# Performance work log

Hardware: AMD Instinct MI355X
Metric: run time of the kernel (lower is better)

Reference implementation:

```python
import jax, jax.numpy as jnp
import numpy as np

EPS = 1e-5

def conv1x1(x, w, b):
    # x: [B,C,H,W], w: [O,C], b: [O]
    return jnp.einsum('bchw,oc->bohw', x, w) + b[None, :, None, None]

def bn(x, g, b, m, v):
    # eval-mode BatchNorm2d over channel axis 1
    s = g / jnp.sqrt(v + EPS)
    return (x - m[None, :, None, None]) * s[None, :, None, None] + b[None, :, None, None]

def setup_inputs() -> dict:
    key = jax.random.key(0)
    ks = jax.random.split(key, 12)
    B, C, Ci, H, W = 8, 512, 256, 64, 64
    d = {}
    d['x'] = jax.random.normal(ks[0], (B, C, H, W), jnp.float32)
    d['theta_w'] = jax.random.normal(ks[1], (Ci, C), jnp.float32) * (C ** -0.5)
    d['theta_b'] = jnp.zeros((Ci,), jnp.float32)
    d['theta_bn_g'] = jax.random.uniform(ks[2], (Ci,), jnp.float32, 0.5, 1.5)
    d['theta_bn_b'] = jax.random.normal(ks[3], (Ci,), jnp.float32) * 0.1
    d['theta_bn_m'] = jnp.zeros((Ci,), jnp.float32)
    d['theta_bn_v'] = jnp.ones((Ci,), jnp.float32)
    d['phi_w'] = jax.random.normal(ks[4], (Ci, C), jnp.float32) * (C ** -0.5)
    d['phi_b'] = jnp.zeros((Ci,), jnp.float32)
    d['phi_bn_g'] = jax.random.uniform(ks[5], (Ci,), jnp.float32, 0.5, 1.5)
    d['phi_bn_b'] = jax.random.normal(ks[6], (Ci,), jnp.float32) * 0.1
    d['phi_bn_m'] = jnp.zeros((Ci,), jnp.float32)
    d['phi_bn_v'] = jnp.ones((Ci,), jnp.float32)
    d['g_w'] = jax.random.normal(ks[7], (Ci, C), jnp.float32) * (C ** -0.5)
    d['g_b'] = jnp.zeros((Ci,), jnp.float32)
    d['wz_w'] = jax.random.normal(ks[8], (C, Ci), jnp.float32) * (Ci ** -0.5)
    d['wz_b'] = jnp.zeros((C,), jnp.float32)
    d['wz_bn_g'] = jax.random.uniform(ks[9], (C,), jnp.float32, 0.5, 1.5)
    d['wz_bn_b'] = jax.random.normal(ks[10], (C,), jnp.float32) * 0.1
    d['wz_bn_m'] = jnp.zeros((C,), jnp.float32)
    d['wz_bn_v'] = jnp.ones((C,), jnp.float32)
    return d

def reference(x, theta_w, theta_b, theta_bn_g, theta_bn_b, theta_bn_m, theta_bn_v,
              phi_w, phi_b, phi_bn_g, phi_bn_b, phi_bn_m, phi_bn_v,
              g_w, g_b, wz_w, wz_b, wz_bn_g, wz_bn_b, wz_bn_m, wz_bn_v):
    B, C, H, W = x.shape
    Ci = theta_w.shape[0]
    N = H * W
    scale = Ci ** -0.5
    th = bn(conv1x1(x, theta_w, theta_b), theta_bn_g, theta_bn_b, theta_bn_m, theta_bn_v).reshape(B, Ci, N)
    ph = bn(conv1x1(x, phi_w, phi_b), phi_bn_g, phi_bn_b, phi_bn_m, phi_bn_v).reshape(B, Ci, N)
    gx = conv1x1(x, g_w, g_b).reshape(B, Ci, N)
    # attn[b,n,m] = <theta[:,n], phi[:,m]> * scale, softmax over m (fp32 as in source)
    attn = jax.nn.softmax(jnp.einsum('bcn,bcm->bnm', th, ph) * scale, axis=-1)
    y = jnp.einsum('bnm,bcm->bcn', attn, gx).reshape(B, Ci, H, W)
    out = bn(conv1x1(y, wz_w, wz_b), wz_bn_g, wz_bn_b, wz_bn_m, wz_bn_v) + x
    return out
```

## Files before the change

kernel.cpp:

```cpp
#include <hip/hip_runtime.h>

typedef __attribute__((ext_vector_type(8))) short bf16x8;
typedef __attribute__((ext_vector_type(4))) float f32x4;
typedef __attribute__((ext_vector_type(16))) float f32x16;
typedef __attribute__((ext_vector_type(4))) unsigned short us4;
typedef __attribute__((ext_vector_type(8))) unsigned short us8;
typedef __attribute__((ext_vector_type(4))) unsigned int u32x4;

#define B_  8
#define C_  512
#define CI_ 256
#define N_  4096

__device__ __forceinline__ unsigned short f2b(float f) {
  unsigned u = __float_as_uint(f);
  u += 0x7FFFu + ((u >> 16) & 1u);
  return (unsigned short)(u >> 16);
}

__device__ __forceinline__ f32x4 mfma16(bf16x8 a, bf16x8 b, f32x4 c) {
  return __builtin_amdgcn_mfma_f32_16x16x32_bf16(a, b, c, 0, 0, 0);
}
__device__ __forceinline__ f32x16 mfma32(bf16x8 a, bf16x8 b, f32x16 c) {
  return __builtin_amdgcn_mfma_f32_32x32x16_bf16(a, b, c, 0, 0, 0);
}

__device__ __forceinline__ void gld16(const void* g, void* l) {
  __builtin_amdgcn_global_load_lds(
      (const __attribute__((address_space(1))) unsigned int*)g,
      (__attribute__((address_space(3))) unsigned int*)l, 16, 0, 0);
}

__global__ void fold_kernel(
  const float* __restrict__ thw, const float* __restrict__ thb,
  const float* __restrict__ thg, const float* __restrict__ thbb,
  const float* __restrict__ thm, const float* __restrict__ thv,
  const float* __restrict__ phw, const float* __restrict__ phb,
  const float* __restrict__ phg, const float* __restrict__ phbb,
  const float* __restrict__ phm, const float* __restrict__ phv,
  const float* __restrict__ gw,  const float* __restrict__ gb,
  const float* __restrict__ wzw, const float* __restrict__ wzb,
  const float* __restrict__ wzg, const float* __restrict__ wzbb,
  const float* __restrict__ wzm, const float* __restrict__ wzv,
  unsigned short* __restrict__ thW, unsigned short* __restrict__ phW,
  unsigned short* __restrict__ gW,  unsigned short* __restrict__ wzW,
  float* __restrict__ bTh, float* __restrict__ bPh,
  float* __restrict__ bG,  float* __restrict__ bWz)
{
  int i = blockIdx.x * 256 + threadIdx.x;
  const int WSZ = CI_ * C_;
  if (i < WSZ) { int o = i >> 9; thW[i] = f2b(thw[i] * (thg[o] * rsqrtf(thv[o] + 1e-5f))); return; }
  i -= WSZ;
  if (i < WSZ) { int o = i >> 9; phW[i] = f2b(phw[i] * (phg[o] * rsqrtf(phv[o] + 1e-5f))); return; }
  i -= WSZ;
  if (i < WSZ) { gW[i] = f2b(gw[i]); return; }
  i -= WSZ;
  if (i < WSZ) { int o = i >> 8; wzW[i] = f2b(wzw[i] * (wzg[o] * rsqrtf(wzv[o] + 1e-5f))); return; }
  i -= WSZ;
  if (i < CI_) { float s = thg[i] * rsqrtf(thv[i] + 1e-5f); bTh[i] = (thb[i] - thm[i]) * s + thbb[i]; return; }
  i -= CI_;
  if (i < CI_) { float s = phg[i] * rsqrtf(phv[i] + 1e-5f); bPh[i] = (phb[i] - phm[i]) * s + phbb[i]; return; }
  i -= CI_;
  if (i < CI_) { bG[i] = gb[i]; return; }
  i -= CI_;
  if (i < C_)  { float s = wzg[i] * rsqrtf(wzv[i] + 1e-5f); bWz[i] = (wzb[i] - wzm[i]) * s + wzbb[i]; return; }
}

__global__ __launch_bounds__(256) void transpose_cast(
  const float* __restrict__ x, unsigned short* __restrict__ xT)
{
  __shared__ float tl[64][68];
  const int b = blockIdx.z, c0 = blockIdx.y * 64, n0 = blockIdx.x * 64;
  const int t = threadIdx.x;
  const int r = t >> 2, q = (t & 3) * 16;
  const float* src = x + ((size_t)(b * C_ + c0 + r)) * N_ + n0 + q;
#pragma unroll
  for (int i = 0; i < 4; i++)
    *(f32x4*)&tl[r][q + i * 4] = *(const f32x4*)(src + i * 4);
  __syncthreads();
  unsigned short* dst = xT + ((size_t)(b * N_ + n0 + r)) * C_ + c0 + q;
  us8 o0, o1;
#pragma unroll
  for (int i = 0; i < 8; i++) o0[i] = f2b(tl[q + i][r]);
#pragma unroll
  for (int i = 0; i < 8; i++) o1[i] = f2b(tl[q + 8 + i][r]);
  *(us8*)dst = o0;
  *(us8*)(dst + 8) = o1;
}

template <int MODE>
__global__ __launch_bounds__(256) void gemm_bt(
  const unsigned short* __restrict__ A,
  const unsigned short* __restrict__ Bm,
  const float* __restrict__ bias,
  const float* __restrict__ resid,
  void* __restrict__ outp,
  int Mdim, int Ndim, int Kdim)
{
  __shared__ unsigned short Al[128][72];
  __shared__ unsigned short Bl[128][72];
  const int b = blockIdx.z;
  const int m0 = blockIdx.y * 128;
  const int n0 = blockIdx.x * 128;
  const int t = threadIdx.x;
  const int w = t >> 6, l = t & 63, l15 = l & 15, g = l >> 4;
  const int wm = w >> 1, wn = w & 1;
  const unsigned short* Bb = Bm + (size_t)b * Ndim * Kdim;
  f32x4 acc[4][4];
#pragma unroll
  for (int i = 0; i < 4; i++)
#pragma unroll
    for (int j = 0; j < 4; j++) acc[i][j] = (f32x4){0.f, 0.f, 0.f, 0.f};

  const int srow = t >> 1, sc = (t & 1) * 4;
  for (int k0 = 0; k0 < Kdim; k0 += 64) {
    __syncthreads();
    const unsigned short* sa = A  + (size_t)(m0 + srow) * Kdim + k0;
    const unsigned short* sb = Bb + (size_t)(n0 + srow) * Kdim + k0;
#pragma unroll
    for (int i = 0; i < 4; i++) {
      int c = (sc + i) * 8;
      *(bf16x8*)&Al[srow][c] = *(const bf16x8*)(sa + c);
      *(bf16x8*)&Bl[srow][c] = *(const bf16x8*)(sb + c);
    }
    __syncthreads();
#pragma unroll
    for (int ks = 0; ks < 2; ks++) {
      bf16x8 af[4], bfr[4];
#pragma unroll
      for (int i = 0; i < 4; i++) af[i]  = *(const bf16x8*)&Al[wm * 64 + i * 16 + l15][ks * 32 + g * 8];
#pragma unroll
      for (int j = 0; j < 4; j++) bfr[j] = *(const bf16x8*)&Bl[wn * 64 + j * 16 + l15][ks * 32 + g * 8];
#pragma unroll
      for (int i = 0; i < 4; i++)
#pragma unroll
        for (int j = 0; j < 4; j++)
          acc[i][j] = mfma16(af[i], bfr[j], acc[i][j]);
    }
  }

#pragma unroll
  for (int i = 0; i < 4; i++) {
    int mrow = m0 + wm * 64 + i * 16 + 4 * g;
    f32x4 b4 = *(const f32x4*)&bias[mrow];
#pragma unroll
    for (int j = 0; j < 4; j++) {
      int n = n0 + wn * 64 + j * 16 + l15;
      f32x4 v = acc[i][j];
      v += b4;
      if constexpr (MODE == 0) {
        us4 pk = { f2b(v[0]), f2b(v[1]), f2b(v[2]), f2b(v[3]) };
        *(us4*)((unsigned short*)outp + ((size_t)b * Ndim + n) * Mdim + mrow) = pk;
      } else if constexpr (MODE == 1) {
        unsigned short* o = (unsigned short*)outp + ((size_t)b * Mdim + mrow) * (size_t)Ndim + n;
#pragma unroll
        for (int jj = 0; jj < 4; jj++) o[(size_t)jj * Ndim] = f2b(v[jj]);
      } else {
        size_t base = ((size_t)b * Mdim + mrow) * (size_t)Ndim + n;
        float* o = (float*)outp;
#pragma unroll
        for (int jj = 0; jj < 4; jj++)
          o[base + (size_t)jj * Ndim] = v[jj] + resid[base + (size_t)jj * Ndim];
      }
    }
  }
}

__global__ __launch_bounds__(256, 1) void attn_kernel(
  const unsigned short* __restrict__ thT,
  const unsigned short* __restrict__ phT,
  const unsigned short* __restrict__ gx,
  unsigned short* __restrict__ yT)
{
  __shared__ __align__(16) unsigned char lds[131072];
  const int t = threadIdx.x;
  const int w = t >> 6, l = t & 63, l31 = l & 31, h = l >> 5;
  const int e7 = l31 & 7;
  const int id = blockIdx.x;
  const int b = id & 7;
  const int n0 = (id >> 3) * 128;
  const unsigned short* thB = thT + (size_t)b * N_ * CI_;
  const unsigned short* phB = phT + (size_t)b * N_ * CI_;
  const unsigned short* gxB = gx  + (size_t)b * CI_ * N_;

  const int kq = l >> 5, kc = l & 31;
  int koff[8];
#pragma unroll
  for (int i = 0; i < 8; i++) {
    int row = w * 16 + 2 * i + kq;
    koff[i] = row * 256 + ((kc ^ (row & 7)) * 8);
  }
  const int vq = l >> 3, vc = l & 7;
  int voff[8];
#pragma unroll
  for (int i = 0; i < 8; i++) {
    int ci = w * 64 + i * 8 + vq;
    voff[i] = ci * 4096 + ((vc ^ (vq & 7)) * 8);
  }

#define STAGE(bufv, m0v) do { \
    const unsigned short* kg_ = phB + (size_t)(m0v) * 256; \
    const unsigned short* vg_ = gxB + (m0v); \
    unsigned kb_ = (unsigned)(bufv) * 65536u + (unsigned)w * 8192u; \
    _Pragma("unroll") \
    for (int i_ = 0; i_ < 8; i_++) \
      gld16(kg_ + koff[i_], lds + kb_ + i_ * 1024); \
    _Pragma("unroll") \
    for (int i_ = 0; i_ < 8; i_++) \
      gld16(vg_ + voff[i_], lds + kb_ + 32768u + i_ * 1024); \
  } while (0)

  bf16x8 q[16];
  {
    const unsigned short* qp = thB + (size_t)(n0 + w * 32 + l31) * CI_ + h * 8;
#pragma unroll
    for (int ks = 0; ks < 16; ks++) q[ks] = *(const bf16x8*)(qp + ks * 16);
  }

  f32x16 acc[8];
#pragma unroll
  for (int i = 0; i < 8; i++)
#pragma unroll
    for (int r = 0; r < 16; r++) acc[i][r] = 0.f;
  float M = -1e30f, L = 0.f;
  const float kS = 0.0625f * 1.44269504f;

  STAGE(0, 0);
  __syncthreads();
  int cur = 0;

  for (int m0 = 0; m0 < N_; m0 += 64) {
    if (m0 + 64 < N_) STAGE(cur ^ 1, m0 + 64);
    const unsigned char* kb = lds + cur * 65536;
    const unsigned char* vb = kb + 32768;

    f32x16 S0, S1;
#pragma unroll
    for (int r = 0; r < 16; r++) { S0[r] = 0.f; S1[r] = 0.f; }
#pragma unroll
    for (int ks = 0; ks < 16; ks++) {
      int col = ((ks * 2 + h) ^ e7) << 4;
      bf16x8 k0 = *(const bf16x8*)(kb + l31 * 512 + col);
      bf16x8 k1 = *(const bf16x8*)(kb + (32 + l31) * 512 + col);
      S0 = mfma32(k0, q[ks], S0);
      S1 = mfma32(k1, q[ks], S1);
    }

    float pm = -1e30f;
#pragma unroll
    for (int r = 0; r < 16; r++) { pm = fmaxf(pm, S0[r]); pm = fmaxf(pm, S1[r]); }
    pm *= kS;
    pm = fmaxf(pm, __shfl_xor(pm, 32));
    int dfr = __all(pm <= M + 8.0f);
    if (!dfr) {
      float nm = fmaxf(M, pm);
      float rs = exp2f(M - nm);
      M = nm; L *= rs;
#pragma unroll
      for (int r = 0; r < 16; r++) {
        float rr = __shfl(rs, h * 32 + ((r & 3) + 8 * (r >> 2) + 4 * h));
#pragma unroll
        for (int c = 0; c < 8; c++) acc[c][r] *= rr;
      }
    }
    float p0[16], p1[16];
    float rsum = 0.f;
#pragma unroll
    for (int r = 0; r < 16; r++) {
      p0[r] = exp2f(S0[r] * kS - M);
      p1[r] = exp2f(S1[r] * kS - M);
      rsum += p0[r] + p1[r];
    }
    rsum += __shfl_xor(rsum, 32);
    L += rsum;

    unsigned pk0[8], pk1[8];
#pragma unroll
    for (int qq = 0; qq < 8; qq++) {
      pk0[qq] = ((unsigned)f2b(p0[2 * qq + 1]) << 16) | f2b(p0[2 * qq]);
      pk1[qq] = ((unsigned)f2b(p1[2 * qq + 1]) << 16) | f2b(p1[2 * qq]);
    }

#pragma unroll
    for (int ks = 0; ks < 4; ks++) {
      const int kp = ks & 1;
      unsigned sel0_0, sel1_0, sel0_1, sel1_1;
      if (ks < 2) {
        sel0_0 = pk0[kp * 4 + 0]; sel1_0 = pk0[kp * 4 + 2];
        sel0_1 = pk0[kp * 4 + 1]; sel1_1 = pk0[kp * 4 + 3];
      } else {
        sel0_0 = pk1[kp * 4 + 0]; sel1_0 = pk1[kp * 4 + 2];
        sel0_1 = pk1[kp * 4 + 1]; sel1_1 = pk1[kp * 4 + 3];
      }
      unsigned own0 = h ? sel1_0 : sel0_0;
      unsigned snd0 = h ? sel0_0 : sel1_0;
      unsigned own1 = h ? sel1_1 : sel0_1;
      unsigned snd1 = h ? sel0_1 : sel1_1;
      unsigned sw0 = (unsigned)__shfl_xor((int)snd0, 32);
      unsigned sw1 = (unsigned)__shfl_xor((int)snd1, 32);
      u32x4 pv;
      pv[0] = h ? sw0 : own0;
      pv[1] = h ? sw1 : own1;
      pv[2] = h ? own0 : sw0;
      pv[3] = h ? own1 : sw1;
      bf16x8 pa = *(bf16x8*)&pv;
      int col = ((ks * 2 + h) ^ e7) << 4;
#pragma unroll
      for (int cit = 0; cit < 8; cit++) {
        bf16x8 vf = *(const bf16x8*)(vb + (cit * 32 + l31) * 128 + col);
        acc[cit] = mfma32(pa, vf, acc[cit]);
      }
    }
    __syncthreads();
    cur ^= 1;
  }

  float inv = 1.0f / L;
  unsigned short* yB = yT + (size_t)b * N_ * CI_;
#pragma unroll
  for (int r = 0; r < 16; r++) {
    int nl = (r & 3) + 8 * (r >> 2) + 4 * h;
    float ir = __shfl(inv, h * 32 + nl);
    int n = n0 + w * 32 + nl;
#pragma unroll
    for (int cit = 0; cit < 8; cit++)
      yB[(size_t)n * CI_ + cit * 32 + l31] = f2b(acc[cit][r] * ir);
  }
#undef STAGE
}

extern "C" void kernel_launch(void* const* d_in, const int* in_sizes, int n_in,
                              void* d_out, int out_size, void* d_ws, size_t ws_size,
                              hipStream_t stream)
{
  const float* x    = (const float*)d_in[0];
  const float* thw  = (const float*)d_in[1];
  const float* thb  = (const float*)d_in[2];
  const float* thg  = (const float*)d_in[3];
  const float* thbb = (const float*)d_in[4];
  const float* thm  = (const float*)d_in[5];
  const float* thv  = (const float*)d_in[6];
  const float* phw  = (const float*)d_in[7];
  const float* phb  = (const float*)d_in[8];
  const float* phg  = (const float*)d_in[9];
  const float* phbb = (const float*)d_in[10];
  const float* phm  = (const float*)d_in[11];
  const float* phv  = (const float*)d_in[12];
  const float* gw   = (const float*)d_in[13];
  const float* gb   = (const float*)d_in[14];
  const float* wzw  = (const float*)d_in[15];
  const float* wzb  = (const float*)d_in[16];
  const float* wzg  = (const float*)d_in[17];
  const float* wzbb = (const float*)d_in[18];
  const float* wzm  = (const float*)d_in[19];
  const float* wzv  = (const float*)d_in[20];

  char* ws = (char*)d_ws;
  unsigned short* xbT = (unsigned short*)(ws);
  unsigned short* thT = (unsigned short*)(ws + 33554432ull);
  unsigned short* phT = (unsigned short*)(ws + 50331648ull);
  unsigned short* gxb = (unsigned short*)(ws + 67108864ull);
  unsigned short* yT  = (unsigned short*)(ws + 83886080ull);
  unsigned short* thW = (unsigned short*)(ws + 100663296ull);
  unsigned short* phW = (unsigned short*)(ws + 100925440ull);
  unsigned short* gW  = (unsigned short*)(ws + 101187584ull);
  unsigned short* wzW = (unsigned short*)(ws + 101449728ull);
  float* bTh = (float*)(ws + 101711872ull);
  float* bPh = (float*)(ws + 101712896ull);
  float* bG  = (float*)(ws + 101713920ull);
  float* bWz = (float*)(ws + 101714944ull);

  fold_kernel<<<2053, 256, 0, stream>>>(
      thw, thb, thg, thbb, thm, thv,
      phw, phb, phg, phbb, phm, phv,
      gw, gb, wzw, wzb, wzg, wzbb, wzm, wzv,
      thW, phW, gW, wzW, bTh, bPh, bG, bWz);

  transpose_cast<<<dim3(64, 8, 8), 256, 0, stream>>>(x, xbT);

  gemm_bt<0><<<dim3(32, 2, 8), 256, 0, stream>>>(thW, xbT, bTh, nullptr, thT, CI_, N_, C_);
  gemm_bt<0><<<dim3(32, 2, 8), 256, 0, stream>>>(phW, xbT, bPh, nullptr, phT, CI_, N_, C_);
  gemm_bt<1><<<dim3(32, 2, 8), 256, 0, stream>>>(gW,  xbT, bG,  nullptr, gxb, CI_, N_, C_);

  attn_kernel<<<dim3(256), 256, 0, stream>>>(thT, phT, gxb, yT);

  gemm_bt<2><<<dim3(32, 4, 8), 256, 0, stream>>>(wzW, yT, bWz, x, d_out, C_, N_, CI_);
}
```

Measured before the change: 325.9 us.

## Split attention KV tiles across two wave groups with LDS merge of softmax partials

The attention kernel moves from 4 waves to 8 waves per block. Each group of 4 waves processes half of every 64-key tile (split-K within the tile), keeping its own running max, sum and accumulator. At the end, the second group writes its partial accumulators and M/L statistics to LDS, and the first group merges them with rescaling before writing the output. This doubles the waves available to hide latency and halves the per-wave QK work, at the cost of a final LDS reduction, extra registers per block, and more LDS (135 KB), which still limits the kernel to one block per CU.

After: 295.6 us. 9.3% less time.

```diff
diff --git a/kernel.cpp b/kernel.cpp
--- a/kernel.cpp
+++ b/kernel.cpp
@@ -166,15 +166,16 @@
   }
 }
 
-__global__ __launch_bounds__(256, 1) void attn_kernel(
+__global__ __launch_bounds__(512, 2) void attn_kernel(
   const unsigned short* __restrict__ thT,
   const unsigned short* __restrict__ phT,
   const unsigned short* __restrict__ gx,
   unsigned short* __restrict__ yT)
 {
-  __shared__ __align__(16) unsigned char lds[131072];
+  __shared__ __align__(16) unsigned char lds[135168];
   const int t = threadIdx.x;
   const int w = t >> 6, l = t & 63, l31 = l & 31, h = l >> 5;
+  const int qt = w & 3, mh = w >> 2;
   const int e7 = l31 & 7;
   const int id = blockIdx.x;
   const int b = id & 7;
@@ -184,35 +185,35 @@
   const unsigned short* gxB = gx  + (size_t)b * CI_ * N_;
 
   const int kq = l >> 5, kc = l & 31;
-  int koff[8];
-#pragma unroll
-  for (int i = 0; i < 8; i++) {
-    int row = w * 16 + 2 * i + kq;
+  int koff[4];
+#pragma unroll
+  for (int i = 0; i < 4; i++) {
+    int row = w * 8 + 2 * i + kq;
     koff[i] = row * 256 + ((kc ^ (row & 7)) * 8);
   }
   const int vq = l >> 3, vc = l & 7;
-  int voff[8];
-#pragma unroll
-  for (int i = 0; i < 8; i++) {
-    int ci = w * 64 + i * 8 + vq;
-    voff[i] = ci * 4096 + ((vc ^ (vq & 7)) * 8);
+  int voff[4];
+#pragma unroll
+  for (int i = 0; i < 4; i++) {
+    int ci = w * 32 + i * 8 + vq;
+    voff[i] = ci * 4096 + ((vc ^ vq) * 8);
   }
 
 #define STAGE(bufv, m0v) do { \
     const unsigned short* kg_ = phB + (size_t)(m0v) * 256; \
     const unsigned short* vg_ = gxB + (m0v); \
-    unsigned kb_ = (unsigned)(bufv) * 65536u + (unsigned)w * 8192u; \
+    unsigned base_ = (unsigned)(bufv) * 65536u + (unsigned)w * 4096u; \
     _Pragma("unroll") \
-    for (int i_ = 0; i_ < 8; i_++) \
-      gld16(kg_ + koff[i_], lds + kb_ + i_ * 1024); \
+    for (int i_ = 0; i_ < 4; i_++) \
+      gld16(kg_ + koff[i_], lds + base_ + i_ * 1024); \
     _Pragma("unroll") \
-    for (int i_ = 0; i_ < 8; i_++) \
-      gld16(vg_ + voff[i_], lds + kb_ + 32768u + i_ * 1024); \
+    for (int i_ = 0; i_ < 4; i_++) \
+      gld16(vg_ + voff[i_], lds + base_ + 32768u + i_ * 1024); \
   } while (0)
 
   bf16x8 q[16];
   {
-    const unsigned short* qp = thB + (size_t)(n0 + w * 32 + l31) * CI_ + h * 8;
+    const unsigned short* qp = thB + (size_t)(n0 + qt * 32 + l31) * CI_ + h * 8;
 #pragma unroll
     for (int ks = 0; ks < 16; ks++) q[ks] = *(const bf16x8*)(qp + ks * 16);
   }
@@ -229,26 +230,24 @@
   __syncthreads();
   int cur = 0;
 
-  for (int m0 = 0; m0 < N_; m0 += 64) {
-    if (m0 + 64 < N_) STAGE(cur ^ 1, m0 + 64);
+  for (int tt = 0; tt < 64; tt++) {
+    const int m0 = tt * 64;
+    if (tt < 63) STAGE(cur ^ 1, m0 + 64);
     const unsigned char* kb = lds + cur * 65536;
     const unsigned char* vb = kb + 32768;
 
-    f32x16 S0, S1;
-#pragma unroll
-    for (int r = 0; r < 16; r++) { S0[r] = 0.f; S1[r] = 0.f; }
+    f32x16 S;
+#pragma unroll
+    for (int r = 0; r < 16; r++) S[r] = 0.f;
 #pragma unroll
     for (int ks = 0; ks < 16; ks++) {
-      int col = ((ks * 2 + h) ^ e7) << 4;
-      bf16x8 k0 = *(const bf16x8*)(kb + l31 * 512 + col);
-      bf16x8 k1 = *(const bf16x8*)(kb + (32 + l31) * 512 + col);
-      S0 = mfma32(k0, q[ks], S0);
-      S1 = mfma32(k1, q[ks], S1);
-    }
-
-    float pm = -1e30f;
-#pragma unroll
-    for (int r = 0; r < 16; r++) { pm = fmaxf(pm, S0[r]); pm = fmaxf(pm, S1[r]); }
+      bf16x8 kf = *(const bf16x8*)(kb + (mh * 32 + l31) * 512 + ((((ks * 2 + h)) ^ e7) << 4));
+      S = mfma32(kf, q[ks], S);
+    }
+
+    float pm = S[0];
+#pragma unroll
+    for (int r = 1; r < 16; r++) pm = fmaxf(pm, S[r]);
     pm *= kS;
     pm = fmaxf(pm, __shfl_xor(pm, 32));
     int dfr = __all(pm <= M + 8.0f);
@@ -263,39 +262,29 @@
         for (int c = 0; c < 8; c++) acc[c][r] *= rr;
       }
     }
-    float p0[16], p1[16];
+    float p[16];
     float rsum = 0.f;
 #pragma unroll
     for (int r = 0; r < 16; r++) {
-      p0[r] = exp2f(S0[r] * kS - M);
-      p1[r] = exp2f(S1[r] * kS - M);
-      rsum += p0[r] + p1[r];
+      p[r] = exp2f(S[r] * kS - M);
+      rsum += p[r];
     }
     rsum += __shfl_xor(rsum, 32);
     L += rsum;
 
-    unsigned pk0[8], pk1[8];
-#pragma unroll
-    for (int qq = 0; qq < 8; qq++) {
-      pk0[qq] = ((unsigned)f2b(p0[2 * qq + 1]) << 16) | f2b(p0[2 * qq]);
-      pk1[qq] = ((unsigned)f2b(p1[2 * qq + 1]) << 16) | f2b(p1[2 * qq]);
-    }
-
-#pragma unroll
-    for (int ks = 0; ks < 4; ks++) {
-      const int kp = ks & 1;
-      unsigned sel0_0, sel1_0, sel0_1, sel1_1;
-      if (ks < 2) {
-        sel0_0 = pk0[kp * 4 + 0]; sel1_0 = pk0[kp * 4 + 2];
-        sel0_1 = pk0[kp * 4 + 1]; sel1_1 = pk0[kp * 4 + 3];
-      } else {
-        sel0_0 = pk1[kp * 4 + 0]; sel1_0 = pk1[kp * 4 + 2];
-        sel0_1 = pk1[kp * 4 + 1]; sel1_1 = pk1[kp * 4 + 3];
-      }
-      unsigned own0 = h ? sel1_0 : sel0_0;
-      unsigned snd0 = h ? sel0_0 : sel1_0;
-      unsigned own1 = h ? sel1_1 : sel0_1;
-      unsigned snd1 = h ? sel0_1 : sel1_1;
+    unsigned pk[8];
+#pragma unroll
+    for (int qq = 0; qq < 8; qq++)
+      pk[qq] = ((unsigned)f2b(p[2 * qq + 1]) << 16) | f2b(p[2 * qq]);
+
+#pragma unroll
+    for (int ks = 0; ks < 2; ks++) {
+      unsigned s00 = pk[ks * 4 + 0], s10 = pk[ks * 4 + 2];
+      unsigned s01 = pk[ks * 4 + 1], s11 = pk[ks * 4 + 3];
+      unsigned own0 = h ? s10 : s00;
+      unsigned snd0 = h ? s00 : s10;
+      unsigned own1 = h ? s11 : s01;
+      unsigned snd1 = h ? s01 : s11;
       unsigned sw0 = (unsigned)__shfl_xor((int)snd0, 32);
       unsigned sw1 = (unsigned)__shfl_xor((int)snd1, 32);
       u32x4 pv;
@@ -304,10 +293,10 @@
       pv[2] = h ? own0 : sw0;
       pv[3] = h ? own1 : sw1;
       bf16x8 pa = *(bf16x8*)&pv;
-      int col = ((ks * 2 + h) ^ e7) << 4;
+      const int gidx = mh * 4 + ks * 2 + h;
 #pragma unroll
       for (int cit = 0; cit < 8; cit++) {
-        bf16x8 vf = *(const bf16x8*)(vb + (cit * 32 + l31) * 128 + col);
+        bf16x8 vf = *(const bf16x8*)(vb + (cit * 32 + l31) * 128 + ((gidx ^ e7) << 4));
         acc[cit] = mfma32(pa, vf, acc[cit]);
       }
     }
@@ -315,16 +304,38 @@
     cur ^= 1;
   }
 
-  float inv = 1.0f / L;
-  unsigned short* yB = yT + (size_t)b * N_ * CI_;
-#pragma unroll
-  for (int r = 0; r < 16; r++) {
-    int nl = (r & 3) + 8 * (r >> 2) + 4 * h;
-    float ir = __shfl(inv, h * 32 + nl);
-    int n = n0 + w * 32 + nl;
+  float* MB = (float*)(lds + 131072);
+  float* LB = (float*)(lds + 131072 + 2048);
+  MB[mh * 256 + qt * 64 + l] = M;
+  LB[mh * 256 + qt * 64 + l] = L;
+  float* ab = (float*)lds + qt * 8192 + l;
+  if (mh) {
 #pragma unroll
     for (int cit = 0; cit < 8; cit++)
-      yB[(size_t)n * CI_ + cit * 32 + l31] = f2b(acc[cit][r] * ir);
+#pragma unroll
+      for (int r = 0; r < 16; r++)
+        ab[(cit * 16 + r) * 64] = acc[cit][r];
+  }
+  __syncthreads();
+  if (!mh) {
+    unsigned short* yB = yT + (size_t)b * N_ * CI_;
+#pragma unroll
+    for (int r = 0; r < 16; r++) {
+      int nl = (r & 3) + 8 * (r >> 2) + 4 * h;
+      int li = qt * 64 + h * 32 + nl;
+      float M1 = MB[li], L1 = LB[li];
+      float M2 = MB[256 + li], L2 = LB[256 + li];
+      float Mf = fmaxf(M1, M2);
+      float s1 = exp2f(M1 - Mf), s2 = exp2f(M2 - Mf);
+      float invf = 1.0f / (L1 * s1 + L2 * s2);
+      s1 *= invf; s2 *= invf;
+      int n = n0 + qt * 32 + nl;
+#pragma unroll
+      for (int cit = 0; cit < 8; cit++) {
+        float v = acc[cit][r] * s1 + ab[(cit * 16 + r) * 64] * s2;
+        yB[(size_t)n * CI_ + cit * 32 + l31] = f2b(v);
+      }
+    }
   }
 #undef STAGE
 }
@@ -382,7 +393,7 @@
   gemm_bt<0><<<dim3(32, 2, 8), 256, 0, stream>>>(phW, xbT, bPh, nullptr, phT, CI_, N_, C_);
   gemm_bt<1><<<dim3(32, 2, 8), 256, 0, stream>>>(gW,  xbT, bG,  nullptr, gxb, CI_, N_, C_);
 
-  attn_kernel<<<dim3(256), 256, 0, stream>>>(thT, phT, gxb, yT);
+  attn_kernel<<<dim3(256), 512, 0, stream>>>(thT, phT, gxb, yT);
 
   gemm_bt<2><<<dim3(32, 4, 8), 256, 0, stream>>>(wzW, yT, bWz, x, d_out, C_, N_, CI_);
 }
```
